# Kernel tuning notes

Hardware: AMD Instinct MI355X
Metric: run time of the kernel (lower is better)

The kernel has to match this reference:

```python
import jax, jax.numpy as jnp
import numpy as np

CLASS_NUM = 31
KERNEL_NUM = 5
KERNEL_MUL = 2.0


def setup_inputs() -> dict:
    key = jax.random.key(0)
    k1, k2, k3, k4 = jax.random.split(key, 4)
    B, D = 4096, 256
    source = jax.random.normal(k1, (B, D), dtype=jnp.float32)
    target = jax.random.normal(k2, (B, D), dtype=jnp.float32)
    s_label = jax.random.randint(k3, (B,), 0, CLASS_NUM, dtype=jnp.int64)
    t_label = jax.random.uniform(k4, (B, CLASS_NUM), dtype=jnp.float32)
    return {"source": source, "target": target, "s_label": s_label, "t_label": t_label}


def _cal_weight(s_label, t_label):
    # Source: one-hot, column-normalized (empty classes -> divide by 100)
    s_onehot = jax.nn.one_hot(s_label, CLASS_NUM, dtype=jnp.float32)
    s_cnt = jnp.sum(s_onehot, axis=0)
    s_vec = s_onehot / jnp.where(s_cnt == 0, 100.0, s_cnt)
    # Target: soft probs, column-normalized (detached in original)
    t_prob = jax.lax.stop_gradient(t_label)
    t_cnt = jnp.sum(t_prob, axis=0)
    t_vec = t_prob / jnp.where(t_cnt == 0, 100.0, t_cnt)
    # Classes present in BOTH source labels and target argmax predictions
    t_arg = jnp.argmax(t_prob, axis=1)
    t_present = jnp.sum(jax.nn.one_hot(t_arg, CLASS_NUM, dtype=jnp.float32), axis=0) > 0
    mask = ((s_cnt > 0) & t_present).astype(jnp.float32)
    n_idx = jnp.maximum(jnp.sum(mask), 1.0)
    s_vec = s_vec * mask
    t_vec = t_vec * mask
    w_ss = (s_vec @ s_vec.T) / n_idx
    w_tt = (t_vec @ t_vec.T) / n_idx
    w_st = (s_vec @ t_vec.T) / n_idx
    return w_ss, w_tt, w_st


def reference(source, target, s_label, t_label):
    B = source.shape[0]
    w_ss, w_tt, w_st = _cal_weight(s_label, t_label)

    # Multi-bandwidth RBF kernel over concatenated samples
    total = jnp.concatenate([source, target], axis=0)  # [2B, D]
    sq = jnp.sum(total * total, axis=1)
    l2 = jnp.maximum(sq[:, None] + sq[None, :] - 2.0 * (total @ total.T), 0.0)  # [2B, 2B]

    n = 2 * B
    bw = jnp.sum(jax.lax.stop_gradient(l2)) / float(max(n * n - n, 1))
    bw = jnp.maximum(bw, 1e-6) / (KERNEL_MUL ** (KERNEL_NUM // 2))
    kernels = jnp.zeros_like(l2)
    for i in range(KERNEL_NUM):
        kernels = kernels + jnp.exp(-l2 / jnp.maximum(bw * KERNEL_MUL ** i, 1e-6))

    ss = kernels[:B, :B]
    tt = kernels[B:, B:]
    st = kernels[:B, B:]
    loss = jnp.sum(w_ss * ss + w_tt * tt - 2.0 * w_st * st)
    return loss
```

## Files before the change

kernel.cpp:

```cpp
#include <hip/hip_runtime.h>
#include <cstddef>


#define B 4096
#define D 256
#define C 31
#define N2 8192
#define NTILE 64
#define NBLK (NTILE * (NTILE + 1) / 2)

typedef __attribute__((ext_vector_type(8))) short bf16x8;
typedef __attribute__((ext_vector_type(4))) float f32x4;

struct WS {
  double sum_sq;
  double Msum[256];
  int s_cnt[32];
  float t_cnt[32];
  int t_pres[32];
  float inv_n_idx;
  float inv_d4;
  float sq[N2];
  int slab[N2];
  float sdv[N2];
  alignas(16) unsigned char Thi8[(size_t)N2 * D];
  alignas(16) unsigned short vhi[(size_t)N2 * 32];
  alignas(16) float v[(size_t)N2 * 32];
  alignas(16) double part[NBLK];
};

static __device__ __forceinline__ unsigned short f2bf(float f) {
  unsigned int u = __float_as_uint(f);
  return (unsigned short)((u + 0x7fffu + ((u >> 16) & 1u)) >> 16);
}
static __device__ __forceinline__ float bf2f(unsigned short s) {
  return __uint_as_float(((unsigned int)s) << 16);
}
static __device__ __forceinline__ float exp2_hw(float x) {
  float r;
  asm("v_exp_f32 %0, %1" : "=v"(r) : "v"(x));
  return r;
}

#define GLD16(gsrc, ldst)                                                     \
  __builtin_amdgcn_global_load_lds(                                           \
      (const __attribute__((address_space(1))) void*)(gsrc),                  \
      (__attribute__((address_space(3))) void*)(ldst), 16, 0, 0)

__global__ void k0_init(WS* __restrict__ ws) {
  int tid = threadIdx.x;
  if (tid == 0) ws->sum_sq = 0.0;
  if (tid < 32) {
    ws->s_cnt[tid] = 0;
    ws->t_cnt[tid] = 0.f;
    ws->t_pres[tid] = 0;
  }
  ws->Msum[tid] = 0.0;
}

__global__ __launch_bounds__(256) void kPrep(const float* __restrict__ src,
                                             const float* __restrict__ tgt,
                                             const int* __restrict__ s_label,
                                             const float* __restrict__ t_label,
                                             WS* __restrict__ ws) {
  int tid = threadIdx.x, w = tid >> 6, lane = tid & 63;
  int r0 = blockIdx.x * 32;
  bool is_src = (r0 < B);
  __shared__ float rsq[32];
  __shared__ float colp[4][256];
  __shared__ int ls[32];
  __shared__ float lt[8][32];
  __shared__ int lpres[32];
  if (tid < 32) { ls[tid] = 0; lpres[tid] = 0; }

  const float* basep =
      is_src ? src + (size_t)r0 * D : tgt + (size_t)(r0 - B) * D;

  float4 xv[8];
#pragma unroll
  for (int i = 0; i < 8; ++i)
    xv[i] = *(const float4*)(basep + (size_t)(w * 8 + i) * D + lane * 4);

  float ca0 = 0.f, ca1 = 0.f, ca2 = 0.f, ca3 = 0.f;
  int sc = lane >> 4, gl = (lane >> 1) & 7, hf = lane & 1;
#pragma unroll
  for (int i = 0; i < 8; ++i) {
    int rr = w * 8 + i;
    int p = r0 + rr;
    float4 x = xv[i];
    unsigned int pk = __builtin_amdgcn_cvt_pk_fp8_f32(x.x, x.y, 0, false);
    pk = __builtin_amdgcn_cvt_pk_fp8_f32(x.z, x.w, pk, true);
    int gp = (gl + p + (p >> 1)) & 7;
    *(unsigned int*)(&ws->Thi8[(size_t)p * D + sc * 64 + gp * 8 + hf * 4]) = pk;
    ca0 += x.x; ca1 += x.y; ca2 += x.z; ca3 += x.w;
    float s = x.x * x.x + x.y * x.y + x.z * x.z + x.w * x.w;
#pragma unroll
    for (int off = 32; off; off >>= 1) s += __shfl_down(s, off, 64);
    if (lane == 0) rsq[rr] = s;
  }
  colp[w][lane * 4 + 0] = ca0;
  colp[w][lane * 4 + 1] = ca1;
  colp[w][lane * 4 + 2] = ca2;
  colp[w][lane * 4 + 3] = ca3;

  if (!is_src) {
    int g = tid >> 5, c = tid & 31;
    float s = 0.f;
    if (c < C) {
#pragma unroll
      for (int k = 0; k < 4; ++k)
        s += t_label[(size_t)(r0 - B + g * 4 + k) * C + c];
    }
    lt[g][c] = s;
    int rr = tid >> 3, j = tid & 7;
    float best = -1e30f;
    int barg = 0;
    for (int c2 = j; c2 < C; c2 += 8) {
      float x = t_label[(size_t)(r0 - B + rr) * C + c2];
      if (x > best) { best = x; barg = c2; }
    }
#pragma unroll
    for (int m = 1; m < 8; m <<= 1) {
      float ob = __shfl_xor(best, m, 64);
      int oa = __shfl_xor(barg, m, 64);
      if (ob > best || (ob == best && oa < barg)) { best = ob; barg = oa; }
    }
    if (j == 0) lpres[barg] = 1;
  }
  __syncthreads();

  if (tid < 32) {
    int p = r0 + tid;
    ws->sq[p] = rsq[tid];
    if (is_src) {
      int lb = s_label[p];
      ws->slab[p] = lb;
      atomicAdd(&ls[lb], 1);
    } else {
      ws->slab[p] = 0;
    }
  }
  if (tid < 64) {
    float ss = (tid < 32) ? rsq[tid] : 0.f;
#pragma unroll
    for (int off = 32; off; off >>= 1) ss += __shfl_down(ss, off, 64);
    if (tid == 0) atomicAdd(&ws->sum_sq, (double)ss);
  }
  atomicAdd(&ws->Msum[tid],
            (double)(colp[0][tid] + colp[1][tid] + colp[2][tid] + colp[3][tid]));
  __syncthreads();
  if (tid < 32) {
    if (is_src) {
      if (ls[tid]) atomicAdd(&ws->s_cnt[tid], ls[tid]);
    } else {
      float s = 0.f;
#pragma unroll
      for (int g = 0; g < 8; ++g) s += lt[g][tid];
      atomicAdd(&ws->t_cnt[tid], s);
      if (lpres[tid]) ws->t_pres[tid] = 1;
    }
  }
}

__global__ __launch_bounds__(256) void kFin(const int* __restrict__ s_label,
                                            const float* __restrict__ t_label,
                                            WS* __restrict__ ws) {
  int tid = threadIdx.x;
  __shared__ float sdiv[32], tdiv[32];
  if (tid < 64) {
    int m = 0;
    if (tid < 32) {
      int cnt = ws->s_cnt[tid];
      m = (tid < C) && (cnt > 0) && (ws->t_pres[tid] != 0);
      sdiv[tid] = m ? 1.f / (float)cnt : 0.f;
      float t = ws->t_cnt[tid];
      tdiv[tid] = m ? 1.f / ((t == 0.f) ? 100.f : t) : 0.f;
    }
    unsigned long long bal = __ballot(m);
    if (tid == 0 && blockIdx.x == 0)
      ws->inv_n_idx = 1.f / fmaxf((float)__popcll(bal), 1.f);
  } else if (tid < 128 && blockIdx.x == 0) {
    int lane = tid - 64;
    double msq = 0.0;
#pragma unroll
    for (int i = 0; i < 4; ++i) {
      double mm = ws->Msum[i * 64 + lane];
      msq += mm * mm;
    }
#pragma unroll
    for (int off = 32; off; off >>= 1) msq += __shfl_down(msq, off, 64);
    if (lane == 0) {
      double S = ws->sum_sq;
      double n = (double)N2;
      double sum_l2 = 2.0 * n * S - 2.0 * msq;
      double bw = sum_l2 / (n * n - n);
      bw = fmax(bw, 1e-6) * 0.25;
      ws->inv_d4 = (float)(1.0 / fmax(bw * 16.0, 1e-6));
    }
  }
  __syncthreads();
  int p = blockIdx.x * 256 + tid;
  float vrow[32];
  if (p < B) {
    int lb = s_label[p];
    float sv = sdiv[lb];
    ws->sdv[p] = sv;
#pragma unroll
    for (int c = 0; c < 32; ++c) vrow[c] = (c == lb) ? sv : 0.f;
  } else {
    ws->sdv[p] = 0.f;
    const float* r = t_label + (size_t)(p - B) * C;
#pragma unroll
    for (int c = 0; c < 32; ++c) vrow[c] = (c < C) ? -r[c] * tdiv[c] : 0.f;
  }
#pragma unroll
  for (int k = 0; k < 8; ++k) {
    float4 vf;
    vf.x = vrow[k * 4 + 0]; vf.y = vrow[k * 4 + 1];
    vf.z = vrow[k * 4 + 2]; vf.w = vrow[k * 4 + 3];
    *(float4*)(&ws->v[(size_t)p * 32 + k * 4]) = vf;
    ushort4 vh;
    vh.x = f2bf(vf.x); vh.y = f2bf(vf.y); vh.z = f2bf(vf.z); vh.w = f2bf(vf.w);
    *(ushort4*)(&ws->vhi[(size_t)p * 32 + k * 4]) = vh;
  }
}

template <int KIND, bool DIAG>
static __device__ __forceinline__ float epi_ss_st(
    const f32x4 (&acc)[4][4], float ci2, const float* tSq, const int* tSlab,
    const float* tSdv, const unsigned short* Vsw, int p0, int q0, int wr,
    int wc, int mrow, int quad) {
  float k2 = 2.f * ci2;
  float cq[4], sdq[4];
  int lq[4];
#pragma unroll
  for (int tj = 0; tj < 4; ++tj) {
    int iq = 128 + wc + tj * 16 + mrow;
    cq[tj] = -ci2 * tSq[iq];
    if (KIND == 0) {
      lq[tj] = tSlab[iq];
      sdq[tj] = tSdv[iq];
    }
  }
  float local = 0.f;
#pragma unroll
  for (int ti = 0; ti < 4; ++ti) {
#pragma unroll
    for (int rg = 0; rg < 4; ++rg) {
      int ip = wr + ti * 16 + quad * 4 + rg;
      float cpl = -ci2 * tSq[ip];
      int lp = tSlab[ip];
      float sp = tSdv[ip];
#pragma unroll
      for (int tj = 0; tj < 4; ++tj) {
        float z = fminf(fmaf(k2, acc[ti][tj][rg], cpl + cq[tj]), 0.f);
        float y = exp2_hw(z);
        float kv = y;
        y *= y; kv += y;
        y *= y; kv += y;
        y *= y; kv += y;
        y *= y; kv += y;
        float wv;
        if (KIND == 0) {
          wv = (lp == lq[tj]) ? sp * sdq[tj] : 0.f;
        } else {
          int ql = wc + tj * 16 + mrow;
          wv = sp * bf2f(Vsw[ql * 32 + ((lp + ql) & 31)]);
        }
        if (DIAG) {
          int p = p0 + ip;
          int q = q0 + wc + tj * 16 + mrow;
          float f = (q > p) ? 2.f : ((q == p) ? 1.f : 0.f);
          local = fmaf(wv * f, kv, local);
        } else {
          local = fmaf(wv, kv, local);
        }
      }
    }
  }
  if (!DIAG) local *= 2.f;
  return local;
}

template <bool DIAG>
static __device__ __forceinline__ float epi_tt(const f32x4 (&acc)[4][4],
                                               float ci2, const float* tSq,
                                               const unsigned short* SA,
                                               const unsigned short* SB,
                                               int p0, int q0, int wr, int wc,
                                               int mrow, int quad) {
  float k2 = 2.f * ci2;
  float cq[4];
#pragma unroll
  for (int tj = 0; tj < 4; ++tj)
    cq[tj] = -ci2 * tSq[128 + wc + tj * 16 + mrow];
  float cp[16];
#pragma unroll
  for (int ti = 0; ti < 4; ++ti)
#pragma unroll
    for (int rg = 0; rg < 4; ++rg)
      cp[ti * 4 + rg] = -ci2 * tSq[wr + ti * 16 + quad * 4 + rg];
  bf16x8 af[4], bfr[4];
#pragma unroll
  for (int ti = 0; ti < 4; ++ti)
    af[ti] = *(const bf16x8*)(SA + (wr + ti * 16 + mrow) * 32 + quad * 8);
#pragma unroll
  for (int tj = 0; tj < 4; ++tj)
    bfr[tj] = *(const bf16x8*)(SB + (wc + tj * 16 + mrow) * 32 + quad * 8);
  float local = 0.f;
#pragma unroll
  for (int ti = 0; ti < 4; ++ti) {
#pragma unroll
    for (int tj = 0; tj < 4; ++tj) {
      f32x4 wv4 = __builtin_amdgcn_mfma_f32_16x16x32_bf16(
          af[ti], bfr[tj], (f32x4){0.f, 0.f, 0.f, 0.f}, 0, 0, 0);
#pragma unroll
      for (int rg = 0; rg < 4; ++rg) {
        float z = fminf(fmaf(k2, acc[ti][tj][rg], cp[ti * 4 + rg] + cq[tj]), 0.f);
        float y = exp2_hw(z);
        float kv = y;
        y *= y; kv += y;
        y *= y; kv += y;
        y *= y; kv += y;
        y *= y; kv += y;
        if (DIAG) {
          int p = p0 + wr + ti * 16 + quad * 4 + rg;
          int q = q0 + wc + tj * 16 + mrow;
          float f = (q > p) ? 2.f : ((q == p) ? 1.f : 0.f);
          local = fmaf(wv4[rg] * f, kv, local);
        } else {
          local = fmaf(wv4[rg], kv, local);
        }
      }
    }
  }
  if (!DIAG) local *= 2.f;
  return local;
}

static __device__ __forceinline__ void do_chunk(const unsigned char* fb,
                                                f32x4 (&acc)[4][4],
                                                const int (&aAdr)[4],
                                                const int (&bAdr)[4]) {
#pragma unroll
  for (int t = 0; t < 2; ++t) {
    const int x = t << 5;
    long aF[4], bF[4];
#pragma unroll
    for (int ti = 0; ti < 4; ++ti)
      aF[ti] = *(const long*)(fb + (aAdr[ti] ^ x));
#pragma unroll
    for (int tj = 0; tj < 4; ++tj)
      bF[tj] = *(const long*)(fb + 8192 + (bAdr[tj] ^ x));
#pragma unroll
    for (int ti = 0; ti < 4; ++ti)
#pragma unroll
      for (int tj = 0; tj < 4; ++tj)
        acc[ti][tj] = __builtin_amdgcn_mfma_f32_16x16x32_fp8_fp8(
            aF[ti], bF[tj], acc[ti][tj], 0, 0, 0);
  }
}

#define WBAR(N)                                                               \
  do {                                                                        \
    asm volatile("s_waitcnt vmcnt(" #N ")" ::: "memory");                     \
    __builtin_amdgcn_s_barrier();                                             \
    asm volatile("" ::: "memory");                                            \
  } while (0)

__global__ __launch_bounds__(256, 3) void k3_main(WS* __restrict__ ws) {
  int tid = threadIdx.x, w = tid >> 6, lane = tid & 63;
  int lin0 = blockIdx.x;
  int e = (lin0 & 7) * (NBLK / 8) + (lin0 >> 3);
  int b = 0, nb = 484, rem = e;
  while (rem >= nb) { rem -= nb; ++b; nb -= 64; }
  int base = b * 8;
  int bq_, r;
  if (rem < 36) {
    bq_ = 0;
    while ((bq_ + 1) * (bq_ + 2) / 2 <= rem) ++bq_;
    r = rem - (bq_ * (bq_ + 1)) / 2;
  } else {
    int t = rem - 36;
    bq_ = 8 + (t >> 3);
    r = t & 7;
  }
  int bp = base + r, bq = base + bq_;
  int p0 = bp * 128, q0 = bq * 128;

  bool is_ss = (bq < 32);
  bool is_tt = (bp >= 32);
  bool is_st = !is_ss && !is_tt;

  __shared__ __align__(16) unsigned char S[3][2][8192];
  __shared__ __align__(16) float tSq[256];
  __shared__ __align__(16) int tSlab[256];
  __shared__ __align__(16) float tSdv[256];
  unsigned short* Vsw = (unsigned short*)&S[1][0][0];
  unsigned short* SA = (unsigned short*)&S[1][0][0];
  unsigned short* SB = (unsigned short*)&S[1][1][0];
  double* red = (double*)&S[2][0][0];

  const int wr = (w >> 1) * 64, wc = (w & 1) * 64;
  const int mrow = lane & 15, quad = lane >> 4;
  f32x4 acc[4][4];
#pragma unroll
  for (int i = 0; i < 4; ++i)
#pragma unroll
    for (int j = 0; j < 4; ++j) acc[i][j] = (f32x4){0.f, 0.f, 0.f, 0.f};

  const unsigned char* T8 = ws->Thi8;
  int rA = tid >> 2, cb16 = (tid & 3) * 16, cp8 = (tid & 3) * 8;
  const unsigned char* a_lo = T8 + (size_t)(p0 + rA) * D + cb16;
  const unsigned char* a_hi = a_lo + (size_t)64 * D;
  const unsigned char* b_lo = T8 + (size_t)(q0 + rA) * D + cb16;
  const unsigned char* b_hi = b_lo + (size_t)64 * D;

#define STAGE(bufi, off)                                                      \
  do {                                                                        \
    GLD16(a_lo + (off), &S[bufi][0][w * 1024]);                               \
    GLD16(a_hi + (off), &S[bufi][0][w * 1024 + 4096]);                        \
    GLD16(b_lo + (off), &S[bufi][1][w * 1024]);                               \
    GLD16(b_hi + (off), &S[bufi][1][w * 1024 + 4096]);                        \
  } while (0)

  int aAdr[4], bAdr[4];
#pragma unroll
  for (int ti = 0; ti < 4; ++ti) {
    int Ra = wr + ti * 16 + mrow;
    aAdr[ti] = Ra * 64 + (((quad + Ra + (Ra >> 1)) & 7) << 3);
    int Rb = wc + ti * 16 + mrow;
    bAdr[ti] = Rb * 64 + (((quad + Rb + (Rb >> 1)) & 7) << 3);
  }

  uint4 stv0 = {0, 0, 0, 0}, stv1 = {0, 0, 0, 0};

  STAGE(0, 0);
  STAGE(1, 64);
  {
    int l32 = lane & 31;
    const float* s1 = ((lane < 32) ? ws->sq + p0 : ws->sq + q0) + l32 * 4;
    GLD16(s1, tSq);
    const int* s2 = ((lane < 32) ? ws->slab + p0 : ws->slab + q0) + l32 * 4;
    GLD16(s2, tSlab);
    const float* s3 = ((lane < 32) ? ws->sdv + p0 : ws->sdv + q0) + l32 * 4;
    GLD16(s3, tSdv);
  }
  WBAR(7);

  STAGE(2, 128);
  do_chunk(&S[0][0][0], acc, aAdr, bAdr);
  WBAR(7);

  STAGE(0, 192);
  do_chunk(&S[1][0][0], acc, aAdr, bAdr);
  WBAR(4);

  if (is_st) {
    const uint4* vsrc = (const uint4*)(ws->vhi + (size_t)(q0 + (tid >> 1)) * 32 +
                                       (tid & 1) * 16);
    stv0 = vsrc[0];
    stv1 = vsrc[1];
  }
  do_chunk(&S[2][0][0], acc, aAdr, bAdr);
  if (is_st) {
    WBAR(2);
  } else {
    WBAR(0);
  }

  if (is_tt) {
    const unsigned short* gA = ws->vhi + (size_t)(p0 + rA) * 32 + cp8;
    const unsigned short* gB = ws->vhi + (size_t)(q0 + rA) * 32 + cp8;
    GLD16(gA, &S[1][0][w * 1024]);
    GLD16(gA + (size_t)64 * 32, &S[1][0][w * 1024 + 4096]);
    GLD16(gB, &S[1][1][w * 1024]);
    GLD16(gB + (size_t)64 * 32, &S[1][1][w * 1024 + 4096]);
  }
  do_chunk(&S[0][0][0], acc, aAdr, bAdr);

  if (is_st) {
    int rr = tid >> 1, h = (tid & 1) * 16;
    unsigned int uu[8] = {stv0.x, stv0.y, stv0.z, stv0.w,
                          stv1.x, stv1.y, stv1.z, stv1.w};
#pragma unroll
    for (int j = 0; j < 8; ++j) {
      Vsw[rr * 32 + ((h + 2 * j + rr) & 31)] = (unsigned short)(uu[j] & 0xffff);
      Vsw[rr * 32 + ((h + 2 * j + 1 + rr) & 31)] = (unsigned short)(uu[j] >> 16);
    }
  }
  __syncthreads();

  float ci2 = ws->inv_d4 * 1.44269504f;
  float local;
  if (is_ss) {
    if (bp == bq)
      local = epi_ss_st<0, true>(acc, ci2, tSq, tSlab, tSdv, Vsw, p0, q0, wr,
                                 wc, mrow, quad);
    else
      local = epi_ss_st<0, false>(acc, ci2, tSq, tSlab, tSdv, Vsw, p0, q0, wr,
                                  wc, mrow, quad);
  } else if (is_st) {
    local = epi_ss_st<1, false>(acc, ci2, tSq, tSlab, tSdv, Vsw, p0, q0, wr,
                                wc, mrow, quad);
  } else {
    if (bp == bq)
      local = epi_tt<true>(acc, ci2, tSq, SA, SB, p0, q0, wr, wc, mrow, quad);
    else
      local = epi_tt<false>(acc, ci2, tSq, SA, SB, p0, q0, wr, wc, mrow, quad);
  }

  double dl = (double)local;
#pragma unroll
  for (int off = 32; off; off >>= 1) dl += __shfl_down(dl, off, 64);
  if (lane == 0) red[w] = dl;
  __syncthreads();
  if (tid == 0) ws->part[lin0] = red[0] + red[1] + red[2] + red[3];
#undef STAGE
}

__global__ __launch_bounds__(256) void k4_out(WS* __restrict__ ws,
                                              float* __restrict__ out) {
  __shared__ double sh[4];
  int tid = threadIdx.x, w = tid >> 6, lane = tid & 63;
  double s = 0.0;
  for (int i = tid; i < NBLK; i += 256) s += ws->part[i];
#pragma unroll
  for (int off = 32; off; off >>= 1) s += __shfl_down(s, off, 64);
  if (lane == 0) sh[w] = s;
  __syncthreads();
  if (tid == 0)
    out[0] = (float)((sh[0] + sh[1] + sh[2] + sh[3]) * (double)ws->inv_n_idx);
}

extern "C" void kernel_launch(void* const* d_in, const int* in_sizes, int n_in,
                              void* d_out, int out_size, void* d_ws, size_t ws_size,
                              hipStream_t stream) {
  const float* src = (const float*)d_in[0];
  const float* tgt = (const float*)d_in[1];
  const int* s_label = (const int*)d_in[2];
  const float* t_label = (const float*)d_in[3];
  float* out = (float*)d_out;
  WS* ws = (WS*)d_ws;

  k0_init<<<1, 256, 0, stream>>>(ws);
  kPrep<<<256, 256, 0, stream>>>(src, tgt, s_label, t_label, ws);
  kFin<<<32, 256, 0, stream>>>(s_label, t_label, ws);
  k3_main<<<NBLK, 256, 0, stream>>>(ws);
  k4_out<<<1, 256, 0, stream>>>(ws, out);
}
```

Measured before the change: 115.2 us.

## Replace atomics with per-block partials and fold final reduction into main kernel

Removes the init kernel by having kPrep write per-block partial sums, counts and presence bitmasks instead of using global atomics, then reduces those partials in kFin. The separate output kernel is removed: the last k3_main block, found through an atomic done counter with threadfences, sums the per-block partials and writes the result. It also stops writing the unused fp32 v array and skips redundant source-row vhi writes. Fewer launches and no atomics are gained, at the cost of a serial 256-iteration Msum reduction in one kFin block and a last-block reduction tail in the main kernel.

```diff
diff --git a/kernel.cpp b/kernel.cpp
--- a/kernel.cpp
+++ b/kernel.cpp
@@ -13,19 +13,19 @@
 typedef __attribute__((ext_vector_type(4))) float f32x4;
 
 struct WS {
-  double sum_sq;
-  double Msum[256];
-  int s_cnt[32];
-  float t_cnt[32];
-  int t_pres[32];
   float inv_n_idx;
   float inv_d4;
+  unsigned done;
+  float pSumsq[256];
+  unsigned pTpres[128];
+  alignas(16) float pMsum[256 * 256];
+  alignas(16) int pScnt[128 * 32];
+  alignas(16) float pTcnt[128 * 32];
   float sq[N2];
   int slab[N2];
   float sdv[N2];
   alignas(16) unsigned char Thi8[(size_t)N2 * D];
   alignas(16) unsigned short vhi[(size_t)N2 * 32];
-  alignas(16) float v[(size_t)N2 * 32];
   alignas(16) double part[NBLK];
 };
 
@@ -46,17 +46,6 @@
   __builtin_amdgcn_global_load_lds(                                           \
       (const __attribute__((address_space(1))) void*)(gsrc),                  \
       (__attribute__((address_space(3))) void*)(ldst), 16, 0, 0)
-
-__global__ void k0_init(WS* __restrict__ ws) {
-  int tid = threadIdx.x;
-  if (tid == 0) ws->sum_sq = 0.0;
-  if (tid < 32) {
-    ws->s_cnt[tid] = 0;
-    ws->t_cnt[tid] = 0.f;
-    ws->t_pres[tid] = 0;
-  }
-  ws->Msum[tid] = 0.0;
-}
 
 __global__ __launch_bounds__(256) void kPrep(const float* __restrict__ src,
                                              const float* __restrict__ tgt,
@@ -64,7 +53,8 @@
                                              const float* __restrict__ t_label,
                                              WS* __restrict__ ws) {
   int tid = threadIdx.x, w = tid >> 6, lane = tid & 63;
-  int r0 = blockIdx.x * 32;
+  int blk = blockIdx.x;
+  int r0 = blk * 32;
   bool is_src = (r0 < B);
   __shared__ float rsq[32];
   __shared__ float colp[4][256];
@@ -144,84 +134,117 @@
     float ss = (tid < 32) ? rsq[tid] : 0.f;
 #pragma unroll
     for (int off = 32; off; off >>= 1) ss += __shfl_down(ss, off, 64);
-    if (tid == 0) atomicAdd(&ws->sum_sq, (double)ss);
-  }
-  atomicAdd(&ws->Msum[tid],
-            (double)(colp[0][tid] + colp[1][tid] + colp[2][tid] + colp[3][tid]));
-  __syncthreads();
-  if (tid < 32) {
-    if (is_src) {
-      if (ls[tid]) atomicAdd(&ws->s_cnt[tid], ls[tid]);
-    } else {
+    if (tid == 0) ws->pSumsq[blk] = ss;
+  }
+  ws->pMsum[blk * 256 + tid] =
+      colp[0][tid] + colp[1][tid] + colp[2][tid] + colp[3][tid];
+  __syncthreads();
+  if (is_src) {
+    if (tid < 32) ws->pScnt[blk * 32 + tid] = ls[tid];
+  } else {
+    if (tid < 32) {
       float s = 0.f;
 #pragma unroll
       for (int g = 0; g < 8; ++g) s += lt[g][tid];
-      atomicAdd(&ws->t_cnt[tid], s);
-      if (lpres[tid]) ws->t_pres[tid] = 1;
-    }
-  }
-}
-
-__global__ __launch_bounds__(256) void kFin(const int* __restrict__ s_label,
-                                            const float* __restrict__ t_label,
+      ws->pTcnt[(blk - 128) * 32 + tid] = s;
+    }
+    if (tid < 64) {
+      int bit = (tid < 32) ? lpres[tid] : 0;
+      unsigned long long bal = __ballot(bit != 0);
+      if (tid == 0) ws->pTpres[blk - 128] = (unsigned)bal;
+    }
+  }
+}
+
+__global__ __launch_bounds__(256) void kFin(const float* __restrict__ t_label,
                                             WS* __restrict__ ws) {
-  int tid = threadIdx.x;
+  int tid = threadIdx.x, w = tid >> 6, lane = tid & 63;
   __shared__ float sdiv[32], tdiv[32];
+  __shared__ int rs[8][32];
+  __shared__ float rt[8][32];
+  __shared__ unsigned pm[2];
+  __shared__ double dm[4], dsq[4];
+
+  {
+    int g = tid >> 5, c = tid & 31;
+    int cs = 0;
+    float ts = 0.f;
+#pragma unroll
+    for (int k = 0; k < 16; ++k) {
+      cs += ws->pScnt[(g * 16 + k) * 32 + c];
+      ts += ws->pTcnt[(g * 16 + k) * 32 + c];
+    }
+    rs[g][c] = cs;
+    rt[g][c] = ts;
+  }
+  if (tid < 128) {
+    unsigned m = ws->pTpres[tid];
+#pragma unroll
+    for (int off = 32; off; off >>= 1) m |= __shfl_down(m, off, 64);
+    if ((tid & 63) == 0) pm[tid >> 6] = m;
+  }
+  __syncthreads();
+
   if (tid < 64) {
     int m = 0;
     if (tid < 32) {
-      int cnt = ws->s_cnt[tid];
-      m = (tid < C) && (cnt > 0) && (ws->t_pres[tid] != 0);
+      int cnt = 0;
+      float t = 0.f;
+#pragma unroll
+      for (int g = 0; g < 8; ++g) { cnt += rs[g][tid]; t += rt[g][tid]; }
+      unsigned pres = pm[0] | pm[1];
+      m = (tid < C) && (cnt > 0) && ((pres >> tid) & 1u);
       sdiv[tid] = m ? 1.f / (float)cnt : 0.f;
-      float t = ws->t_cnt[tid];
       tdiv[tid] = m ? 1.f / ((t == 0.f) ? 100.f : t) : 0.f;
     }
     unsigned long long bal = __ballot(m);
     if (tid == 0 && blockIdx.x == 0)
       ws->inv_n_idx = 1.f / fmaxf((float)__popcll(bal), 1.f);
-  } else if (tid < 128 && blockIdx.x == 0) {
-    int lane = tid - 64;
-    double msq = 0.0;
-#pragma unroll
-    for (int i = 0; i < 4; ++i) {
-      double mm = ws->Msum[i * 64 + lane];
-      msq += mm * mm;
-    }
-#pragma unroll
-    for (int off = 32; off; off >>= 1) msq += __shfl_down(msq, off, 64);
-    if (lane == 0) {
-      double S = ws->sum_sq;
+  }
+
+  if (blockIdx.x == 0) {
+    double m = 0.0;
+    for (int b2 = 0; b2 < 256; ++b2) m += (double)ws->pMsum[b2 * 256 + tid];
+    double msq = m * m;
+    double ssq = (double)ws->pSumsq[tid];
+#pragma unroll
+    for (int off = 32; off; off >>= 1) {
+      msq += __shfl_down(msq, off, 64);
+      ssq += __shfl_down(ssq, off, 64);
+    }
+    if (lane == 0) { dm[w] = msq; dsq[w] = ssq; }
+    __syncthreads();
+    if (tid == 0) {
+      double MSQ = dm[0] + dm[1] + dm[2] + dm[3];
+      double S = dsq[0] + dsq[1] + dsq[2] + dsq[3];
       double n = (double)N2;
-      double sum_l2 = 2.0 * n * S - 2.0 * msq;
+      double sum_l2 = 2.0 * n * S - 2.0 * MSQ;
       double bw = sum_l2 / (n * n - n);
       bw = fmax(bw, 1e-6) * 0.25;
       ws->inv_d4 = (float)(1.0 / fmax(bw * 16.0, 1e-6));
-    }
-  }
-  __syncthreads();
+      ws->done = 0u;
+    }
+  }
+  __syncthreads();
+
   int p = blockIdx.x * 256 + tid;
-  float vrow[32];
   if (p < B) {
-    int lb = s_label[p];
-    float sv = sdiv[lb];
-    ws->sdv[p] = sv;
-#pragma unroll
-    for (int c = 0; c < 32; ++c) vrow[c] = (c == lb) ? sv : 0.f;
+    ws->sdv[p] = sdiv[ws->slab[p]];
   } else {
     ws->sdv[p] = 0.f;
     const float* r = t_label + (size_t)(p - B) * C;
+    float vrow[32];
 #pragma unroll
     for (int c = 0; c < 32; ++c) vrow[c] = (c < C) ? -r[c] * tdiv[c] : 0.f;
-  }
-#pragma unroll
-  for (int k = 0; k < 8; ++k) {
-    float4 vf;
-    vf.x = vrow[k * 4 + 0]; vf.y = vrow[k * 4 + 1];
-    vf.z = vrow[k * 4 + 2]; vf.w = vrow[k * 4 + 3];
-    *(float4*)(&ws->v[(size_t)p * 32 + k * 4]) = vf;
-    ushort4 vh;
-    vh.x = f2bf(vf.x); vh.y = f2bf(vf.y); vh.z = f2bf(vf.z); vh.w = f2bf(vf.w);
-    *(ushort4*)(&ws->vhi[(size_t)p * 32 + k * 4]) = vh;
+#pragma unroll
+    for (int k = 0; k < 8; ++k) {
+      ushort4 vh;
+      vh.x = f2bf(vrow[k * 4 + 0]);
+      vh.y = f2bf(vrow[k * 4 + 1]);
+      vh.z = f2bf(vrow[k * 4 + 2]);
+      vh.w = f2bf(vrow[k * 4 + 3]);
+      *(ushort4*)(&ws->vhi[(size_t)p * 32 + k * 4]) = vh;
+    }
   }
 }
 
@@ -368,7 +391,8 @@
     asm volatile("" ::: "memory");                                            \
   } while (0)
 
-__global__ __launch_bounds__(256, 3) void k3_main(WS* __restrict__ ws) {
+__global__ __launch_bounds__(256, 3) void k3_main(WS* __restrict__ ws,
+                                                  float* __restrict__ out) {
   int tid = threadIdx.x, w = tid >> 6, lane = tid & 63;
   int lin0 = blockIdx.x;
   int e = (lin0 & 7) * (NBLK / 8) + (lin0 >> 3);
@@ -396,6 +420,7 @@
   __shared__ __align__(16) float tSq[256];
   __shared__ __align__(16) int tSlab[256];
   __shared__ __align__(16) float tSdv[256];
+  __shared__ unsigned lastf;
   unsigned short* Vsw = (unsigned short*)&S[1][0][0];
   unsigned short* SA = (unsigned short*)&S[1][0][0];
   unsigned short* SB = (unsigned short*)&S[1][1][0];
@@ -515,22 +540,26 @@
   for (int off = 32; off; off >>= 1) dl += __shfl_down(dl, off, 64);
   if (lane == 0) red[w] = dl;
   __syncthreads();
-  if (tid == 0) ws->part[lin0] = red[0] + red[1] + red[2] + red[3];
+  if (tid == 0) {
+    ws->part[lin0] = red[0] + red[1] + red[2] + red[3];
+    __threadfence();
+    unsigned old = atomicAdd(&ws->done, 1u);
+    lastf = (old == NBLK - 1) ? 1u : 0u;
+  }
+  __syncthreads();
+  if (lastf) {
+    __threadfence();
+    double s = 0.0;
+    for (int i = tid; i < NBLK; i += 256) s += ws->part[i];
+#pragma unroll
+    for (int off = 32; off; off >>= 1) s += __shfl_down(s, off, 64);
+    if (lane == 0) red[8 + w] = s;
+    __syncthreads();
+    if (tid == 0)
+      out[0] = (float)((red[8] + red[9] + red[10] + red[11]) *
+                       (double)ws->inv_n_idx);
+  }
 #undef STAGE
-}
-
-__global__ __launch_bounds__(256) void k4_out(WS* __restrict__ ws,
-                                              float* __restrict__ out) {
-  __shared__ double sh[4];
-  int tid = threadIdx.x, w = tid >> 6, lane = tid & 63;
-  double s = 0.0;
-  for (int i = tid; i < NBLK; i += 256) s += ws->part[i];
-#pragma unroll
-  for (int off = 32; off; off >>= 1) s += __shfl_down(s, off, 64);
-  if (lane == 0) sh[w] = s;
-  __syncthreads();
-  if (tid == 0)
-    out[0] = (float)((sh[0] + sh[1] + sh[2] + sh[3]) * (double)ws->inv_n_idx);
 }
 
 extern "C" void kernel_launch(void* const* d_in, const int* in_sizes, int n_in,
@@ -543,9 +572,7 @@
   float* out = (float*)d_out;
   WS* ws = (WS*)d_ws;
 
-  k0_init<<<1, 256, 0, stream>>>(ws);
   kPrep<<<256, 256, 0, stream>>>(src, tgt, s_label, t_label, ws);
-  kFin<<<32, 256, 0, stream>>>(s_label, t_label, ws);
-  k3_main<<<NBLK, 256, 0, stream>>>(ws);
-  k4_out<<<1, 256, 0, stream>>>(ws, out);
-}
+  kFin<<<32, 256, 0, stream>>>(t_label, ws);
+  k3_main<<<NBLK, 256, 0, stream>>>(ws, out);
+}
```

After: 146.7 us. 1.27x slower.
